# Kernel optimization log

Hardware: AMD Instinct MI355X
Metric: run time of the kernel (lower is better)

## Reference

```python
import jax, jax.numpy as jnp
import numpy as np

B, S, M = 8, 2048, 2048
STATE, MEM, DH, DOUT = 1024, 1024, 512, 512
K_CURV = 1.0
BETA = 1.0 / np.sqrt(DH)
EPS = 1e-12
MAX_TAN_NORM = 3.5


def setup_inputs() -> dict:
    key = jax.random.key(0)
    ks = jax.random.split(key, 6)
    return {
        "queries": jax.random.normal(ks[0], (B, S, STATE), jnp.float32),
        "keys": jax.random.normal(ks[1], (B, M, MEM), jnp.float32),
        "values": jax.random.normal(ks[2], (B, M, MEM), jnp.float32),
        "Wq": jax.random.normal(ks[3], (DH, STATE), jnp.float32) * (1.0 / np.sqrt(STATE)),
        "bq": jnp.zeros((DH,), jnp.float32),
        "Wk": jax.random.normal(ks[4], (DH, MEM), jnp.float32) * (1.0 / np.sqrt(MEM)),
        "bk": jnp.zeros((DH,), jnp.float32),
        "Wv": jax.random.normal(ks[5], (DOUT, MEM), jnp.float32) * (1.0 / np.sqrt(MEM)),
        "bv": jnp.zeros((DOUT,), jnp.float32),
    }


def _expmap0(x, k):
    # to_tangent0: [0, x] with norm clamped to <= 3.5 (time component is 0 so norm == ||x||)
    n = jnp.linalg.norm(x, axis=-1, keepdims=True)
    v = x * jnp.minimum(MAX_TAN_NORM / (n + 1e-7), 1.0)
    # exp map at origin o = (1/sqrt(k), 0) of Lorentz model with <x,x>_L = -1/k
    sk = jnp.sqrt(k)
    vn = jnp.maximum(jnp.linalg.norm(v, axis=-1, keepdims=True), EPS)
    th = sk * vn
    x0 = jnp.cosh(th) / sk
    xs = jnp.sinh(th) * v / (sk * vn)
    return jnp.concatenate([x0, xs], axis=-1)  # (..., d+1)


def _forward(queries, keys, values, Wq, bq, Wk, bk, Wv, bv):
    k = jnp.asarray(K_CURV, queries.dtype)
    sk = jnp.sqrt(k)
    Q = _expmap0(queries @ Wq.T + bq, k)  # (B,S,DH+1)
    Kh = _expmap0(keys @ Wk.T + bk, k)    # (B,M,DH+1)
    V = _expmap0(values @ Wv.T + bv, k)   # (B,M,DOUT+1)

    # pairwise Lorentz distance: d(x,y) = arccosh(-k <x,y>_L)/sqrt(k)
    # <x,y>_L = -x0*y0 + xs.ys ; computed as matmul + rank-1 term, no (B,S,M,d) blowup
    inner = jnp.einsum('bsd,bmd->bsm', Q[..., 1:], Kh[..., 1:]) \
            - Q[..., 0][:, :, None] * Kh[..., 0][:, None, :]
    dists = jnp.arccosh(jnp.maximum(-k * inner, 1.0 + 1e-7)) / sk  # (B,S,M)

    alpha = jax.nn.softmax(-BETA * dists, axis=-1)  # (B,S,M)

    # Einstein midpoint aggregation
    v_klein = V[..., 1:] / jnp.maximum(V[..., :1], EPS)                 # (B,M,DOUT)
    vn2 = jnp.minimum(jnp.sum(v_klein * v_klein, -1, keepdims=True), 1.0 - 1e-6)
    gamma = 1.0 / jnp.sqrt(jnp.maximum(1.0 - vn2, EPS))                 # (B,M,1)
    denom = jnp.maximum(jnp.einsum('bsm,bm->bs', alpha, gamma[..., 0]), EPS)[..., None]
    mid = jnp.einsum('bsm,bmd->bsd', alpha, gamma * v_klein) / denom    # (B,S,DOUT)
    mn = jnp.maximum(jnp.linalg.norm(mid, axis=-1, keepdims=True), EPS)
    mid = jnp.where(mn >= 1.0, mid / mn * (1.0 - 1e-6), mid)

    # Klein -> hyperboloid
    mn2 = jnp.minimum(jnp.sum(mid * mid, -1, keepdims=True), 1.0 - 1e-6)
    z0 = 1.0 / jnp.sqrt(jnp.maximum(k * (1.0 - mn2), EPS))
    zs = z0 * mid

    # logmap0 -> Euclidean spatial components
    d0 = jnp.arccosh(jnp.maximum(sk * z0, 1.0 + 1e-7)) / sk
    zsn = jnp.maximum(jnp.linalg.norm(zs, axis=-1, keepdims=True), EPS)
    return d0 * zs / zsn  # (B,S,DOUT)


def reference(queries, keys, values, Wq, bq, Wk, bk, Wv, bv):
    return _forward(queries, keys, values, Wq, bq, Wk, bk, Wv, bv)
```

## Files before the change

### kernel.cpp

```cpp
#include <hip/hip_runtime.h>
#include <hip/hip_bf16.h>
#include <cstdint>
#include <cstddef>


typedef _Float16 f16x8 __attribute__((ext_vector_type(8)));
typedef _Float16 f16x4 __attribute__((ext_vector_type(4)));
typedef float    f32x4 __attribute__((ext_vector_type(4)));

#define BETA_F 0.04419417382415922f
#define LOG2E_F 1.4426950408889634f
#define LN2_F 0.6931471805599453f

__device__ __forceinline__ void gload_lds16(const void* g, void* l) {
  __builtin_amdgcn_global_load_lds(
      (__attribute__((address_space(1))) void*)(g),
      (__attribute__((address_space(3))) void*)(l), 16, 0, 0);
}

#define K1_PIT 40

__global__ __launch_bounds__(256) void k_proj(
    const float* __restrict__ xq, const float* __restrict__ xk, const float* __restrict__ xv,
    const float* __restrict__ wq, const float* __restrict__ wk, const float* __restrict__ wv,
    const float* __restrict__ bq, const float* __restrict__ bk, const float* __restrict__ bv,
    _Float16* __restrict__ proj)
{
  __shared__ __align__(16) _Float16 As[128 * K1_PIT];
  __shared__ __align__(16) _Float16 Bs[128 * K1_PIT];

  const int tid = threadIdx.x;
  const int w = tid >> 6, l = tid & 63, ln = l & 15, q = l >> 4;
  const int wm = w & 1, wn = w >> 1;
  const int r0 = blockIdx.y * 128;
  const int n0 = blockIdx.x * 128;
  const int which = r0 >> 14;
  const int rloc = r0 & 16383;
  const float* X = (which == 0) ? xq : ((which == 1) ? xk : xv);
  const float* W = (which == 0) ? wq : ((which == 1) ? wk : wv);
  const float* bias = (which == 0) ? bq : ((which == 1) ? bk : bv);

  f32x4 acc[4][4];
#pragma unroll
  for (int mt = 0; mt < 4; ++mt)
#pragma unroll
    for (int nt = 0; nt < 4; ++nt) acc[mt][nt] = f32x4{0.f, 0.f, 0.f, 0.f};

  for (int kk = 0; kk < 1024; kk += 32) {
    __syncthreads();
#pragma unroll
    for (int it = 0; it < 4; ++it) {
      int v = tid + 256 * it;
      int row = v >> 3, c4 = v & 7;
      float4 a = *(const float4*)(X + (size_t)(rloc + row) * 1024 + kk + c4 * 4);
      float4 b = *(const float4*)(W + (size_t)(n0 + row) * 1024 + kk + c4 * 4);
      f16x4 ah = { (_Float16)a.x, (_Float16)a.y, (_Float16)a.z, (_Float16)a.w };
      f16x4 bh = { (_Float16)b.x, (_Float16)b.y, (_Float16)b.z, (_Float16)b.w };
      *(f16x4*)&As[row * K1_PIT + c4 * 4] = ah;
      *(f16x4*)&Bs[row * K1_PIT + c4 * 4] = bh;
    }
    __syncthreads();

    f16x8 af[4], bf[4];
#pragma unroll
    for (int mt = 0; mt < 4; ++mt)
      af[mt] = *(const f16x8*)&As[(wm * 64 + mt * 16 + ln) * K1_PIT + q * 8];
#pragma unroll
    for (int nt = 0; nt < 4; ++nt)
      bf[nt] = *(const f16x8*)&Bs[(wn * 64 + nt * 16 + ln) * K1_PIT + q * 8];
#pragma unroll
    for (int mt = 0; mt < 4; ++mt)
#pragma unroll
      for (int nt = 0; nt < 4; ++nt)
        acc[mt][nt] = __builtin_amdgcn_mfma_f32_16x16x32_f16(af[mt], bf[nt], acc[mt][nt], 0, 0, 0);
  }

  float bl[4];
#pragma unroll
  for (int nt = 0; nt < 4; ++nt) bl[nt] = bias[n0 + wn * 64 + nt * 16 + ln];
#pragma unroll
  for (int mt = 0; mt < 4; ++mt)
#pragma unroll
    for (int nt = 0; nt < 4; ++nt)
#pragma unroll
      for (int i = 0; i < 4; ++i) {
        int r = r0 + wm * 64 + mt * 16 + q * 4 + i;
        int c = n0 + wn * 64 + nt * 16 + ln;
        proj[(size_t)r * 512 + c] = (_Float16)(acc[mt][nt][i] + bl[nt]);
      }
}

__global__ __launch_bounds__(256) void k_rowstats(
    const _Float16* __restrict__ proj, float* __restrict__ fs, float* __restrict__ c0)
{
  const int w = threadIdx.x >> 6, l = threadIdx.x & 63;
  const int r = blockIdx.x * 4 + w;
  const f16x8 v = *(const f16x8*)(proj + (size_t)r * 512 + l * 8);
  float ss = 0.f;
#pragma unroll
  for (int j = 0; j < 8; ++j) { float x = (float)v[j]; ss += x * x; }
#pragma unroll
  for (int m = 1; m < 64; m <<= 1) ss += __shfl_xor(ss, m, 64);
  if (l == 0) {
    float n = sqrtf(ss);
    float s = fminf(3.5f / (n + 1e-7f), 1.0f);
    float vn = fmaxf(n * s, 1e-12f);
    float e = __builtin_amdgcn_exp2f(vn * LOG2E_F);
    float ie = 1.0f / e;
    c0[r] = 0.5f * (e + ie);
    fs[r] = 0.5f * (e - ie) * s / vn;
  }
}

#define K2_TP 72

__global__ __launch_bounds__(256) void k_transpose_v(
    const _Float16* __restrict__ proj, _Float16* __restrict__ xvT)
{
  __shared__ __align__(16) unsigned short t[64 * K2_TP];
  const int b = blockIdx.z, m0 = blockIdx.x * 64, d0 = blockIdx.y * 64;
  const unsigned short* pv =
      (const unsigned short*)(proj + (size_t)(32768 + b * 2048 + m0) * 512);
#pragma unroll
  for (int it = 0; it < 2; ++it) {
    int v = threadIdx.x + 256 * it;
    int r = v >> 3, c4 = v & 7;
    uint4 dd = *(const uint4*)(pv + (size_t)r * 512 + d0 + c4 * 8);
    *(uint4*)&t[r * K2_TP + c4 * 8] = dd;
  }
  __syncthreads();
#pragma unroll
  for (int it = 0; it < 2; ++it) {
    int v = threadIdx.x + 256 * it;
    int dr = v >> 3, mc = v & 7;
    unsigned int o[4];
#pragma unroll
    for (int jj = 0; jj < 4; ++jj) {
      unsigned int lo = t[(mc * 8 + jj * 2) * K2_TP + dr];
      unsigned int hi = t[(mc * 8 + jj * 2 + 1) * K2_TP + dr];
      o[jj] = lo | (hi << 16);
    }
    uint4 dd = { o[0], o[1], o[2], o[3] };
    unsigned short* dst =
        (unsigned short*)(xvT + ((size_t)b * 512 + d0 + dr) * 2048 + m0 + mc * 8);
    *(uint4*)dst = dd;
  }
}

__global__ __launch_bounds__(256, 2) void k_attn(
    const _Float16* __restrict__ proj, const _Float16* __restrict__ xvT,
    const float* __restrict__ fs, const float* __restrict__ c0,
    float* __restrict__ out)
{
  __shared__ __align__(16) _Float16 KA[16384];
  __shared__ __align__(16) _Float16 KB[16384];
  __shared__ __align__(16) _Float16 P[32 * 40];
  __shared__ float s_den[2][32];
  __shared__ float s_mn2[4][32];
  __shared__ float s_g[32];

  const int tid = threadIdx.x;
  const int w = tid >> 6, l = tid & 63, ln = l & 15, q = l >> 4;
  const int rh = w >> 1, ch = w & 1;
  const int b = blockIdx.y;
  const int s0 = blockIdx.x * 32;

  const _Float16* projq = proj + (size_t)(b * 2048 + s0) * 512;
  const _Float16* projk = proj + (size_t)(16384 + b * 2048) * 512;
  const _Float16* vt = xvT + (size_t)b * 512 * 2048;
  const float* fqp = fs + b * 2048 + s0;
  const float* fkp = fs + 16384 + b * 2048;
  const float* fvp = fs + 32768 + b * 2048;
  const float* cqp = c0 + b * 2048 + s0;
  const float* ckp = c0 + 16384 + b * 2048;
  const float* cvp = c0 + 32768 + b * 2048;

#pragma unroll
  for (int rr = 0; rr < 8; ++rr) {
    int mloc = w * 8 + rr;
    const _Float16* g = projk + (size_t)mloc * 512 + ((l ^ (mloc & 7)) * 8);
    gload_lds16(g, &KA[mloc * 512]);
  }

  f16x8 qf[16];
  {
    const _Float16* qrow = projq + (size_t)(rh * 16 + ln) * 512;
#pragma unroll
    for (int kc = 0; kc < 16; ++kc) qf[kc] = *(const f16x8*)(qrow + kc * 32 + q * 8);
  }
  float cq_i[4], fq_i[4];
#pragma unroll
  for (int i = 0; i < 4; ++i) {
    cq_i[i] = cqp[rh * 16 + q * 4 + i];
    fq_i[i] = fqp[rh * 16 + q * 4 + i];
  }
  const int mll = ch * 16 + ln;
  float ck_c = ckp[mll], fk_c = fkp[mll], fv_c = fvp[mll], cv_c = cvp[mll];

  f32x4 acc[2][8];
#pragma unroll
  for (int rt = 0; rt < 2; ++rt)
#pragma unroll
    for (int nt = 0; nt < 8; ++nt) acc[rt][nt] = f32x4{0.f, 0.f, 0.f, 0.f};
  float den_acc[4] = {0.f, 0.f, 0.f, 0.f};

  for (int m0 = 0; m0 < 2048; m0 += 32) {
    __syncthreads();
#pragma unroll
    for (int uu = 0; uu < 8; ++uu) {
      int u = w * 8 + uu;
      int dloc = u * 16 + (l >> 2);
      int cg = (l & 3) ^ ((dloc >> 1) & 3);
      const _Float16* g = vt + (size_t)dloc * 2048 + m0 + cg * 8;
      gload_lds16(g, &KB[u * 512]);
    }
    float ck_n = 0.f, fk_n = 0.f, fv_n = 0.f, cv_n = 0.f;
    if (m0 + 32 < 2048) {
      int mn = m0 + 32 + ch * 16 + ln;
      ck_n = ckp[mn]; fk_n = fkp[mn]; fv_n = fvp[mn]; cv_n = cvp[mn];
    }

    f32x4 pacc = f32x4{0.f, 0.f, 0.f, 0.f};
    {
      const _Float16* krow = &KA[(ch * 16 + ln) * 512];
      const int msw = (ch * 16 + ln) & 7;
#pragma unroll
      for (int kc = 0; kc < 16; ++kc) {
        f16x8 kf = *(const f16x8*)(krow + (((kc * 4 + q) ^ msw) * 8));
        pacc = __builtin_amdgcn_mfma_f32_16x16x32_f16(qf[kc], kf, pacc, 0, 0, 0);
      }
    }
#pragma unroll
    for (int i = 0; i < 4; ++i) {
      float x = cq_i[i] * ck_c - (fq_i[i] * fk_c) * pacc[i];
      x = fmaxf(x, 1.0f + 1e-7f);
      float r_ = x + __builtin_amdgcn_sqrtf(x * x - 1.0f);
      float p = __builtin_amdgcn_exp2f(-BETA_F * __builtin_amdgcn_logf(r_));
      den_acc[i] += p * cv_c;
      P[(rh * 16 + q * 4 + i) * 40 + ch * 16 + ln] = (_Float16)(p * fv_c);
    }
    __syncthreads();
    if (m0 + 32 < 2048) {
#pragma unroll
      for (int rr = 0; rr < 8; ++rr) {
        int mloc = w * 8 + rr;
        const _Float16* g = projk + (size_t)(m0 + 32 + mloc) * 512 + ((l ^ (mloc & 7)) * 8);
        gload_lds16(g, &KA[mloc * 512]);
      }
    }
#pragma unroll
    for (int rt = 0; rt < 2; ++rt) {
      f16x8 pf = *(const f16x8*)&P[(rt * 16 + ln) * 40 + q * 8];
#pragma unroll
      for (int nt = 0; nt < 8; ++nt) {
        int d = w * 128 + nt * 16 + ln;
        f16x8 vf = *(const f16x8*)&KB[d * 32 + ((q ^ ((d >> 1) & 3)) * 8)];
        acc[rt][nt] = __builtin_amdgcn_mfma_f32_16x16x32_f16(pf, vf, acc[rt][nt], 0, 0, 0);
      }
    }
    ck_c = ck_n; fk_c = fk_n; fv_c = fv_n; cv_c = cv_n;
  }

#pragma unroll
  for (int i = 0; i < 4; ++i) {
    float v = den_acc[i];
    v += __shfl_xor(v, 1, 64); v += __shfl_xor(v, 2, 64);
    v += __shfl_xor(v, 4, 64); v += __shfl_xor(v, 8, 64);
    if (ln == 0) s_den[ch][rh * 16 + q * 4 + i] = v;
  }
  __syncthreads();
  if (tid < 32) {
    float dv = fmaxf(s_den[0][tid] + s_den[1][tid], 1e-12f);
    s_den[0][tid] = 1.0f / dv;
  }
  __syncthreads();
#pragma unroll
  for (int rt = 0; rt < 2; ++rt)
#pragma unroll
    for (int i = 0; i < 4; ++i) {
      int s = rt * 16 + q * 4 + i;
      float inv = s_den[0][s];
      float mm = 0.f;
#pragma unroll
      for (int nt = 0; nt < 8; ++nt) {
        float mid = acc[rt][nt][i] * inv;
        mm += mid * mid;
      }
      mm += __shfl_xor(mm, 1, 64); mm += __shfl_xor(mm, 2, 64);
      mm += __shfl_xor(mm, 4, 64); mm += __shfl_xor(mm, 8, 64);
      if (ln == 0) s_mn2[w][s] = mm;
    }
  __syncthreads();
  if (tid < 32) {
    float mn2 = s_mn2[0][tid] + s_mn2[1][tid] + s_mn2[2][tid] + s_mn2[3][tid];
    float mn = sqrtf(mn2);
    float sc = (mn >= 1.0f) ? (1.0f - 1e-6f) / mn : 1.0f;
    float mn2c = fminf(mn2 * sc * sc, 1.0f - 1e-6f);
    float z0 = 1.0f / sqrtf(fmaxf(1.0f - mn2c, 1e-12f));
    float zc = fmaxf(z0, 1.0f + 1e-7f);
    float d0 = LN2_F * __builtin_amdgcn_logf(zc + __builtin_amdgcn_sqrtf(zc * zc - 1.0f));
    s_g[tid] = (d0 / fmaxf(mn, 1e-12f)) * s_den[0][tid];
  }
  __syncthreads();

  float* pbuf = (float*)KA;
  for (int sp = 0; sp < 16; ++sp) {
#pragma unroll
    for (int rt = 0; rt < 2; ++rt)
#pragma unroll
      for (int i = 0; i < 4; ++i) {
        int s = rt * 16 + q * 4 + i;
        if ((s >> 1) == sp) {
          float gg = s_g[s];
#pragma unroll
          for (int nt = 0; nt < 8; ++nt)
            pbuf[(s & 1) * 512 + w * 128 + nt * 16 + ln] = gg * acc[rt][nt][i];
        }
      }
    __syncthreads();
    {
      int row = tid >> 7, c4 = tid & 127;
      float4 vv = *(float4*)&pbuf[row * 512 + c4 * 4];
      *(float4*)&out[((size_t)(b * 2048 + s0 + sp * 2 + row)) * 512 + c4 * 4] = vv;
    }
    __syncthreads();
  }
}

extern "C" void kernel_launch(void* const* d_in, const int* in_sizes, int n_in,
                              void* d_out, int out_size, void* d_ws, size_t ws_size,
                              hipStream_t stream) {
  (void)in_sizes; (void)n_in; (void)out_size; (void)ws_size;
  const float* xq = (const float*)d_in[0];
  const float* xk = (const float*)d_in[1];
  const float* xv = (const float*)d_in[2];
  const float* wq = (const float*)d_in[3];
  const float* bq = (const float*)d_in[4];
  const float* wk = (const float*)d_in[5];
  const float* bk = (const float*)d_in[6];
  const float* wv = (const float*)d_in[7];
  const float* bv = (const float*)d_in[8];
  float* out = (float*)d_out;
  char* ws = (char*)d_ws;

  _Float16* proj = (_Float16*)(ws);
  _Float16* xvT  = (_Float16*)(ws + 50331648);
  float* fsc     = (float*)(ws + 67108864);
  float* c0a     = (float*)(ws + 67305472);

  k_proj<<<dim3(4, 384), 256, 0, stream>>>(xq, xk, xv, wq, wk, wv, bq, bk, bv, proj);
  k_rowstats<<<dim3(12288), 256, 0, stream>>>(proj, fsc, c0a);
  k_transpose_v<<<dim3(32, 8, 8), 256, 0, stream>>>(proj, xvT);
  k_attn<<<dim3(64, 8), 256, 0, stream>>>(proj, xvT, fsc, c0a, out);
}
```

Before: 465.2 us.

## Double-buffer projection GEMM tiles and remap blocks per XCD for L2 reuse

The projection GEMM now double-buffers its LDS tiles. Global loads for the next K-slice go into registers before the MFMA work on the current slice, and are converted and stored into the other buffer afterward, which leaves one barrier per iteration instead of two. The launch also becomes a 1D grid whose block IDs are remapped so that each XCD handles a contiguous range of row blocks, with all four column blocks sharing the same X rows, to improve L2 locality. In exchange, LDS use doubles and register pressure rises from holding prefetched float4s.

```diff
diff --git a/kernel.cpp b/kernel.cpp
--- a/kernel.cpp
+++ b/kernel.cpp
@@ -26,54 +26,82 @@
     const float* __restrict__ bq, const float* __restrict__ bk, const float* __restrict__ bv,
     _Float16* __restrict__ proj)
 {
-  __shared__ __align__(16) _Float16 As[128 * K1_PIT];
-  __shared__ __align__(16) _Float16 Bs[128 * K1_PIT];
+  __shared__ __align__(16) _Float16 As[2][128 * K1_PIT];
+  __shared__ __align__(16) _Float16 Bs[2][128 * K1_PIT];
 
   const int tid = threadIdx.x;
   const int w = tid >> 6, l = tid & 63, ln = l & 15, q = l >> 4;
   const int wm = w & 1, wn = w >> 1;
-  const int r0 = blockIdx.y * 128;
-  const int n0 = blockIdx.x * 128;
+
+  const int id = blockIdx.x;
+  const int xcd = id & 7, j = id >> 3;
+  const int rowblk = xcd * 48 + (j >> 2);
+  const int colblk = j & 3;
+  const int r0 = rowblk * 128;
+  const int n0 = colblk * 128;
   const int which = r0 >> 14;
   const int rloc = r0 & 16383;
   const float* X = (which == 0) ? xq : ((which == 1) ? xk : xv);
   const float* W = (which == 0) ? wq : ((which == 1) ? wk : wv);
   const float* bias = (which == 0) ? bq : ((which == 1) ? bk : bv);
 
+  const int lrow = tid >> 3, lc4 = tid & 7;
+  const float* Xb = X + (size_t)(rloc + lrow) * 1024 + lc4 * 4;
+  const float* Wb = W + (size_t)(n0 + lrow) * 1024 + lc4 * 4;
+
   f32x4 acc[4][4];
 #pragma unroll
   for (int mt = 0; mt < 4; ++mt)
 #pragma unroll
     for (int nt = 0; nt < 4; ++nt) acc[mt][nt] = f32x4{0.f, 0.f, 0.f, 0.f};
 
+  float4 ar[4], br[4];
+#define K1_LOAD(kk)                                                      \
+  {                                                                      \
+    _Pragma("unroll") for (int it = 0; it < 4; ++it) {                   \
+      ar[it] = *(const float4*)(Xb + (size_t)(32 * it) * 1024 + (kk));   \
+      br[it] = *(const float4*)(Wb + (size_t)(32 * it) * 1024 + (kk));   \
+    }                                                                    \
+  }
+#define K1_STORE(buf)                                                    \
+  {                                                                      \
+    _Pragma("unroll") for (int it = 0; it < 4; ++it) {                   \
+      int row = lrow + 32 * it;                                          \
+      f16x4 ah = { (_Float16)ar[it].x, (_Float16)ar[it].y,               \
+                   (_Float16)ar[it].z, (_Float16)ar[it].w };             \
+      f16x4 bh = { (_Float16)br[it].x, (_Float16)br[it].y,               \
+                   (_Float16)br[it].z, (_Float16)br[it].w };             \
+      *(f16x4*)&As[buf][row * K1_PIT + lc4 * 4] = ah;                    \
+      *(f16x4*)&Bs[buf][row * K1_PIT + lc4 * 4] = bh;                    \
+    }                                                                    \
+  }
+
+  K1_LOAD(0);
+  K1_STORE(0);
+  int cur = 0;
+
   for (int kk = 0; kk < 1024; kk += 32) {
     __syncthreads();
-#pragma unroll
-    for (int it = 0; it < 4; ++it) {
-      int v = tid + 256 * it;
-      int row = v >> 3, c4 = v & 7;
-      float4 a = *(const float4*)(X + (size_t)(rloc + row) * 1024 + kk + c4 * 4);
-      float4 b = *(const float4*)(W + (size_t)(n0 + row) * 1024 + kk + c4 * 4);
-      f16x4 ah = { (_Float16)a.x, (_Float16)a.y, (_Float16)a.z, (_Float16)a.w };
-      f16x4 bh = { (_Float16)b.x, (_Float16)b.y, (_Float16)b.z, (_Float16)b.w };
-      *(f16x4*)&As[row * K1_PIT + c4 * 4] = ah;
-      *(f16x4*)&Bs[row * K1_PIT + c4 * 4] = bh;
-    }
-    __syncthreads();
+    if (kk + 32 < 1024) K1_LOAD(kk + 32);
 
     f16x8 af[4], bf[4];
 #pragma unroll
     for (int mt = 0; mt < 4; ++mt)
-      af[mt] = *(const f16x8*)&As[(wm * 64 + mt * 16 + ln) * K1_PIT + q * 8];
+      af[mt] = *(const f16x8*)&As[cur][(wm * 64 + mt * 16 + ln) * K1_PIT + q * 8];
 #pragma unroll
     for (int nt = 0; nt < 4; ++nt)
-      bf[nt] = *(const f16x8*)&Bs[(wn * 64 + nt * 16 + ln) * K1_PIT + q * 8];
+      bf[nt] = *(const f16x8*)&Bs[cur][(wn * 64 + nt * 16 + ln) * K1_PIT + q * 8];
 #pragma unroll
     for (int mt = 0; mt < 4; ++mt)
 #pragma unroll
       for (int nt = 0; nt < 4; ++nt)
         acc[mt][nt] = __builtin_amdgcn_mfma_f32_16x16x32_f16(af[mt], bf[nt], acc[mt][nt], 0, 0, 0);
-  }
+
+    if (kk + 32 < 1024) K1_STORE(cur ^ 1);
+    cur ^= 1;
+  }
+#undef K1_LOAD
+#undef K1_STORE
 
   float bl[4];
 #pragma unroll
@@ -348,7 +376,7 @@
   float* fsc     = (float*)(ws + 67108864);
   float* c0a     = (float*)(ws + 67305472);
 
-  k_proj<<<dim3(4, 384), 256, 0, stream>>>(xq, xk, xv, wq, wk, wv, bq, bk, bv, proj);
+  k_proj<<<dim3(1536), 256, 0, stream>>>(xq, xk, xv, wq, wk, wv, bq, bk, bv, proj);
   k_rowstats<<<dim3(12288), 256, 0, stream>>>(proj, fsc, c0a);
   k_transpose_v<<<dim3(32, 8, 8), 256, 0, stream>>>(proj, xvT);
   k_attn<<<dim3(64, 8), 256, 0, stream>>>(proj, xvT, fsc, c0a, out);
```

After: 460.4 us. Within noise of the previous version (-1.0%).

## Pre-convert projection inputs to fp16 and double-buffer async LDS loads in GEMM

Applied to the files above, without the earlier changes.

The projection GEMM no longer converts fp32 to fp16 while staging tiles. Weights and each input tensor are first converted to fp16 by separate elementwise kernels, using the output buffer and a workspace region as scratch. The GEMM then streams fp16 tiles into double-buffered LDS with direct global-to-LDS loads and an XOR swizzle, and remaps blocks so each XCD handles contiguous rows. This adds extra conversion passes and kernel launches plus scratch traffic, in exchange for halving GEMM global reads and overlapping loads with MFMA.

```diff
diff --git a/kernel.cpp b/kernel.cpp
--- a/kernel.cpp
+++ b/kernel.cpp
@@ -18,62 +18,98 @@
       (__attribute__((address_space(3))) void*)(l), 16, 0, 0);
 }
 
-#define K1_PIT 40
-
-__global__ __launch_bounds__(256) void k_proj(
-    const float* __restrict__ xq, const float* __restrict__ xk, const float* __restrict__ xv,
-    const float* __restrict__ wq, const float* __restrict__ wk, const float* __restrict__ wv,
-    const float* __restrict__ bq, const float* __restrict__ bk, const float* __restrict__ bv,
-    _Float16* __restrict__ proj)
-{
-  __shared__ __align__(16) _Float16 As[128 * K1_PIT];
-  __shared__ __align__(16) _Float16 Bs[128 * K1_PIT];
+__global__ __launch_bounds__(256) void k_cvt_w(
+    const float* __restrict__ wq, const float* __restrict__ wk,
+    const float* __restrict__ wv, _Float16* __restrict__ wh)
+{
+  size_t cid = (size_t)blockIdx.x * 256 + threadIdx.x;
+  int m = (int)(cid >> 16);
+  size_t off = (cid & 65535) << 3;
+  const float* src = (m == 0 ? wq : (m == 1 ? wk : wv)) + off;
+  float4 a = *(const float4*)src;
+  float4 b = *(const float4*)(src + 4);
+  f16x8 h = { (_Float16)a.x, (_Float16)a.y, (_Float16)a.z, (_Float16)a.w,
+              (_Float16)b.x, (_Float16)b.y, (_Float16)b.z, (_Float16)b.w };
+  *(f16x8*)(wh + (cid << 3)) = h;
+}
+
+__global__ __launch_bounds__(256) void k_cvt_x(
+    const float* __restrict__ src, _Float16* __restrict__ dst)
+{
+  size_t cid = (size_t)blockIdx.x * 256 + threadIdx.x;
+  const float* s = src + (cid << 3);
+  float4 a = *(const float4*)s;
+  float4 b = *(const float4*)(s + 4);
+  f16x8 h = { (_Float16)a.x, (_Float16)a.y, (_Float16)a.z, (_Float16)a.w,
+              (_Float16)b.x, (_Float16)b.y, (_Float16)b.z, (_Float16)b.w };
+  *(f16x8*)(dst + (cid << 3)) = h;
+}
+
+__global__ __launch_bounds__(256, 4) void k_proj(
+    const _Float16* __restrict__ xh, const _Float16* __restrict__ wh,
+    const float* __restrict__ bias, _Float16* __restrict__ proj)
+{
+  __shared__ __align__(16) _Float16 Ab[2][128 * 32];
+  __shared__ __align__(16) _Float16 Bb[2][128 * 32];
 
   const int tid = threadIdx.x;
   const int w = tid >> 6, l = tid & 63, ln = l & 15, q = l >> 4;
   const int wm = w & 1, wn = w >> 1;
-  const int r0 = blockIdx.y * 128;
-  const int n0 = blockIdx.x * 128;
-  const int which = r0 >> 14;
-  const int rloc = r0 & 16383;
-  const float* X = (which == 0) ? xq : ((which == 1) ? xk : xv);
-  const float* W = (which == 0) ? wq : ((which == 1) ? wk : wv);
-  const float* bias = (which == 0) ? bq : ((which == 1) ? bk : bv);
+
+  const int id = blockIdx.x;
+  const int xcd = id & 7, j = id >> 3;
+  const int rowblk = xcd * 16 + (j >> 2);
+  const int colblk = j & 3;
+  const int r0 = rowblk * 128;
+  const int n0 = colblk * 128;
+  const _Float16* Xrow = xh + (size_t)r0 * 1024;
+  const _Float16* Wrow = wh + (size_t)n0 * 1024;
+
+  const int srr = l >> 2, ss = l & 3;
 
   f32x4 acc[4][4];
 #pragma unroll
   for (int mt = 0; mt < 4; ++mt)
 #pragma unroll
     for (int nt = 0; nt < 4; ++nt) acc[mt][nt] = f32x4{0.f, 0.f, 0.f, 0.f};
+
+#define K1_STAGE(buf, kk)                                                    \
+  {                                                                          \
+    _Pragma("unroll") for (int i = 0; i < 2; ++i) {                          \
+      int ar = (i * 4 + w) * 16 + srr;                                       \
+      gload_lds16(Xrow + (size_t)ar * 1024 + (kk) + ((ss ^ (ar & 3)) << 3),  \
+                  &Ab[buf][(i * 4 + w) * 512]);                              \
+      gload_lds16(Wrow + (size_t)ar * 1024 + (kk) + ((ss ^ (ar & 3)) << 3),  \
+                  &Bb[buf][(i * 4 + w) * 512]);                              \
+    }                                                                        \
+  }
+
+  K1_STAGE(0, 0);
+  int cur = 0;
 
   for (int kk = 0; kk < 1024; kk += 32) {
     __syncthreads();
-#pragma unroll
-    for (int it = 0; it < 4; ++it) {
-      int v = tid + 256 * it;
-      int row = v >> 3, c4 = v & 7;
-      float4 a = *(const float4*)(X + (size_t)(rloc + row) * 1024 + kk + c4 * 4);
-      float4 b = *(const float4*)(W + (size_t)(n0 + row) * 1024 + kk + c4 * 4);
-      f16x4 ah = { (_Float16)a.x, (_Float16)a.y, (_Float16)a.z, (_Float16)a.w };
-      f16x4 bh = { (_Float16)b.x, (_Float16)b.y, (_Float16)b.z, (_Float16)b.w };
-      *(f16x4*)&As[row * K1_PIT + c4 * 4] = ah;
-      *(f16x4*)&Bs[row * K1_PIT + c4 * 4] = bh;
-    }
-    __syncthreads();
+    if (kk + 32 < 1024) K1_STAGE(cur ^ 1, kk + 32);
 
     f16x8 af[4], bf[4];
 #pragma unroll
-    for (int mt = 0; mt < 4; ++mt)
-      af[mt] = *(const f16x8*)&As[(wm * 64 + mt * 16 + ln) * K1_PIT + q * 8];
-#pragma unroll
-    for (int nt = 0; nt < 4; ++nt)
-      bf[nt] = *(const f16x8*)&Bs[(wn * 64 + nt * 16 + ln) * K1_PIT + q * 8];
+    for (int mt = 0; mt < 4; ++mt) {
+      int ar = wm * 64 + mt * 16 + ln;
+      af[mt] = *(const f16x8*)&Ab[cur][ar * 32 + ((q ^ (ar & 3)) << 3)];
+    }
+#pragma unroll
+    for (int nt = 0; nt < 4; ++nt) {
+      int br = wn * 64 + nt * 16 + ln;
+      bf[nt] = *(const f16x8*)&Bb[cur][br * 32 + ((q ^ (br & 3)) << 3)];
+    }
 #pragma unroll
     for (int mt = 0; mt < 4; ++mt)
 #pragma unroll
       for (int nt = 0; nt < 4; ++nt)
         acc[mt][nt] = __builtin_amdgcn_mfma_f32_16x16x32_f16(af[mt], bf[nt], acc[mt][nt], 0, 0, 0);
-  }
+    cur ^= 1;
+  }
+#undef K1_STAGE
 
   float bl[4];
 #pragma unroll
@@ -345,10 +381,21 @@
 
   _Float16* proj = (_Float16*)(ws);
   _Float16* xvT  = (_Float16*)(ws + 50331648);
+  _Float16* wh   = (_Float16*)(ws + 50331648);
   float* fsc     = (float*)(ws + 67108864);
   float* c0a     = (float*)(ws + 67305472);
-
-  k_proj<<<dim3(4, 384), 256, 0, stream>>>(xq, xk, xv, wq, wk, wv, bq, bk, bv, proj);
+  _Float16* xs   = (_Float16*)d_out;
+
+  k_cvt_w<<<dim3(768), 256, 0, stream>>>(wq, wk, wv, wh);
+
+  const float* xsrc[3] = { xq, xk, xv };
+  const float* bsrc[3] = { bq, bk, bv };
+  for (int p = 0; p < 3; ++p) {
+    k_cvt_x<<<dim3(8192), 256, 0, stream>>>(xsrc[p], xs);
+    k_proj<<<dim3(512), 256, 0, stream>>>(
+        xs, wh + (size_t)p * 512 * 1024, bsrc[p], proj + (size_t)p * 16384 * 512);
+  }
+
   k_rowstats<<<dim3(12288), 256, 0, stream>>>(proj, fsc, c0a);
   k_transpose_v<<<dim3(32, 8, 8), 256, 0, stream>>>(proj, xvT);
   k_attn<<<dim3(64, 8), 256, 0, stream>>>(proj, xvT, fsc, c0a, out);
```

Result: faster. 448.6 us (-3.6%).
